# Performance work log

Hardware: AMD Instinct MI355X
Metric: run time of the kernel (lower is better)

Reference implementation:

```python
import jax, jax.numpy as jnp
import numpy as np

EMBED_DIM = 2048
HEAD_DIM = 128


def setup_inputs() -> dict:
    key = jax.random.key(0)
    ks = jax.random.split(key, 7)
    B, S = 4, 2048
    lim = 1.0 / np.sqrt(EMBED_DIM)
    hidden_state = jax.random.normal(ks[0], (B, S, EMBED_DIM), dtype=jnp.float32)
    # nn.Linear weights stored as [out, in]; we keep [in, out] for x @ W
    Wq = jax.random.uniform(ks[1], (EMBED_DIM, HEAD_DIM), minval=-lim, maxval=lim, dtype=jnp.float32)
    Wk = jax.random.uniform(ks[2], (EMBED_DIM, HEAD_DIM), minval=-lim, maxval=lim, dtype=jnp.float32)
    Wv = jax.random.uniform(ks[3], (EMBED_DIM, HEAD_DIM), minval=-lim, maxval=lim, dtype=jnp.float32)
    bq = jax.random.uniform(ks[4], (HEAD_DIM,), minval=-lim, maxval=lim, dtype=jnp.float32)
    bk = jax.random.uniform(ks[5], (HEAD_DIM,), minval=-lim, maxval=lim, dtype=jnp.float32)
    bv = jax.random.uniform(ks[6], (HEAD_DIM,), minval=-lim, maxval=lim, dtype=jnp.float32)
    return {"hidden_state": hidden_state, "Wq": Wq, "bq": bq, "Wk": Wk, "bk": bk, "Wv": Wv, "bv": bv}


def reference(hidden_state, Wq, bq, Wk, bk, Wv, bv):
    q = hidden_state @ Wq + bq  # [B,S,D]
    k = hidden_state @ Wk + bk
    v = hidden_state @ Wv + bv
    scale = 1.0 / jnp.sqrt(jnp.asarray(HEAD_DIM, dtype=q.dtype))
    scores = jnp.einsum("bqd,bkd->bqk", q, k) * scale  # [B,S,S]
    S = q.shape[1]
    causal = jnp.triu(jnp.ones((S, S), dtype=bool), k=1)
    scores = jnp.where(causal, jnp.asarray(-1e10, dtype=scores.dtype), scores)
    weights = jax.nn.softmax(scores, axis=-1)
    return jnp.einsum("bqk,bkd->bqd", weights, v)
```

## Files before the change

### kernel.cpp

```cpp
#include <hip/hip_runtime.h>
#include <hip/hip_bf16.h>

#define EMBED 2048
#define SEQ   2048
#define BATCH 4
#define HD    128
#define MROWS (BATCH * SEQ)
#define NTOT  (3 * HD)
#define SCALE 0.08838834764831845f
#define NQT   (SEQ / 16)
#define NSPL  2
#define FIXM  4.0f

typedef __attribute__((ext_vector_type(8))) short bf16x8;
typedef __attribute__((ext_vector_type(4))) float f32x4;

__device__ __forceinline__ unsigned short f2bf_rne(float x) {
    union { float f; unsigned u; } c; c.f = x;
    unsigned r = c.u + 0x7fffu + ((c.u >> 16) & 1u);
    return (unsigned short)(r >> 16);
}

#define MFMA16(a, b, c) __builtin_amdgcn_mfma_f32_16x16x32_bf16((a), (b), (c), 0, 0, 0)

__device__ __forceinline__ void gload_lds16(const unsigned short* gp, unsigned short* lp) {
    __builtin_amdgcn_global_load_lds(
        (const __attribute__((address_space(1))) void*)gp,
        (__attribute__((address_space(3))) void*)lp, 16, 0, 0);
}

__global__ __launch_bounds__(256) void h_conv(
    const float* __restrict__ H, unsigned short* __restrict__ Hbf)
{
    const size_t i = ((size_t)blockIdx.x * 256 + threadIdx.x) * 8;
    const float4 f0 = *(const float4*)(H + i);
    const float4 f1 = *(const float4*)(H + i + 4);
    union { unsigned short s[8]; uint4 v; } u;
    u.s[0] = f2bf_rne(f0.x); u.s[1] = f2bf_rne(f0.y);
    u.s[2] = f2bf_rne(f0.z); u.s[3] = f2bf_rne(f0.w);
    u.s[4] = f2bf_rne(f1.x); u.s[5] = f2bf_rne(f1.y);
    u.s[6] = f2bf_rne(f1.z); u.s[7] = f2bf_rne(f1.w);
    *(uint4*)(Hbf + i) = u.v;
}

__global__ __launch_bounds__(256) void wt_conv(
    const float* __restrict__ Wq, const float* __restrict__ Wk,
    const float* __restrict__ Wv, unsigned short* __restrict__ WT)
{
    __shared__ float lds[64][129];
    const int tid = threadIdx.x;
    const int blk = blockIdx.x;
    const int mat = blk >> 5;
    const int k0  = (blk & 31) * 64;
    const float* src = (mat == 0) ? Wq : (mat == 1) ? Wk : Wv;

    const float4* s4 = (const float4*)(src + (size_t)k0 * HD);
    for (int i = tid; i < 2048; i += 256) {
        const float4 v = s4[i];
        const int k  = i >> 5;
        const int n4 = (i & 31) * 4;
        lds[k][n4 + 0] = v.x; lds[k][n4 + 1] = v.y;
        lds[k][n4 + 2] = v.z; lds[k][n4 + 3] = v.w;
    }
    __syncthreads();

    const int n  = tid >> 1;
    const int kc = (tid & 1) * 32;
    unsigned short* dst = WT + ((size_t)(mat * HD + n)) * EMBED + k0 + kc;
#pragma unroll
    for (int c = 0; c < 4; ++c) {
        union { unsigned short s[8]; uint4 v; } u;
#pragma unroll
        for (int i = 0; i < 8; ++i)
            u.s[i] = f2bf_rne(lds[kc + c * 8 + i][n]);
        ((uint4*)dst)[c] = u.v;
    }
}

__global__ __launch_bounds__(256, 2) void gemm_qkv(
    const unsigned short* __restrict__ Hbf, const unsigned short* __restrict__ WT,
    const float* __restrict__ bq, const float* __restrict__ bk,
    const float* __restrict__ bv,
    unsigned short* __restrict__ Qbf, unsigned short* __restrict__ Kbf,
    unsigned short* __restrict__ VT)
{
    __shared__ unsigned short Abuf[128 * 64];
    __shared__ unsigned short Bbuf[64 * 64];

    const int tid  = threadIdx.x;
    const int w    = tid >> 6;
    const int lane = tid & 63;
    const int l16  = lane & 15;
    const int quad = lane >> 4;

    const int bid   = blockIdx.x;
    const int xcd   = bid & 7;
    const int local = bid >> 3;
    const int n_blk = local % 6;
    const int m_grp = local / 6;
    const int m0 = (m_grp * 8 + xcd) * 128;
    const int n0 = n_blk * 64;

    const int lr   = lane >> 3;
    const int slot = lane & 7;
    const int gch  = slot ^ lr;
    const unsigned short* ag[4]; unsigned short* al[4];
#pragma unroll
    for (int t = 0; t < 4; ++t) {
        const int r = (w * 4 + t) * 8 + lr;
        ag[t] = Hbf + (size_t)(m0 + r) * EMBED + gch * 8;
        al[t] = Abuf + (w * 4 + t) * 512;
    }
    const unsigned short* bg[2]; unsigned short* bl[2];
#pragma unroll
    for (int t = 0; t < 2; ++t) {
        const int r = (w * 2 + t) * 8 + lr;
        bg[t] = WT + (size_t)(n0 + r) * EMBED + gch * 8;
        bl[t] = Bbuf + (w * 2 + t) * 512;
    }

    const int wm = (w >> 1) * 64;
    const int wn = (w & 1) * 32;
    const int xq = l16 & 7;

    f32x4 acc[4][2];
#pragma unroll
    for (int mt = 0; mt < 4; ++mt)
#pragma unroll
        for (int nt = 0; nt < 2; ++nt) {
            f32x4 z = {0.f, 0.f, 0.f, 0.f};
            acc[mt][nt] = z;
        }

    for (int kt = 0; kt < EMBED / 64; ++kt) {
        const int ko = kt * 64;
#pragma unroll
        for (int t = 0; t < 4; ++t) gload_lds16(ag[t] + ko, al[t]);
#pragma unroll
        for (int t = 0; t < 2; ++t) gload_lds16(bg[t] + ko, bl[t]);
        __syncthreads();

        bf16x8 aF[4][2], bF[2][2];
#pragma unroll
        for (int mt = 0; mt < 4; ++mt)
#pragma unroll
            for (int ks = 0; ks < 2; ++ks)
                aF[mt][ks] = *(const bf16x8*)(
                    Abuf + (wm + mt * 16 + l16) * 64 + (((ks * 4 + quad) ^ xq) * 8));
#pragma unroll
        for (int nt = 0; nt < 2; ++nt)
#pragma unroll
            for (int ks = 0; ks < 2; ++ks)
                bF[nt][ks] = *(const bf16x8*)(
                    Bbuf + (wn + nt * 16 + l16) * 64 + (((ks * 4 + quad) ^ xq) * 8));
#pragma unroll
        for (int ks = 0; ks < 2; ++ks)
#pragma unroll
            for (int mt = 0; mt < 4; ++mt)
#pragma unroll
                for (int nt = 0; nt < 2; ++nt)
                    acc[mt][nt] = MFMA16(aF[mt][ks], bF[nt][ks], acc[mt][nt]);
        __syncthreads();
    }

#pragma unroll
    for (int nt = 0; nt < 2; ++nt) {
        const int col = n0 + wn + nt * 16 + l16;
        const int sel = col >> 7;
        const int c   = col & (HD - 1);
        const float bias = (sel == 0 ? bq : (sel == 1 ? bk : bv))[c];
#pragma unroll
        for (int mt = 0; mt < 4; ++mt) {
#pragma unroll
            for (int r = 0; r < 4; ++r) {
                const int row = m0 + wm + mt * 16 + quad * 4 + r;
                const float v = acc[mt][nt][r] + bias;
                if (sel == 0) {
                    Qbf[(size_t)row * HD + c] = f2bf_rne(v * SCALE);
                } else if (sel == 1) {
                    Kbf[(size_t)row * HD + c] = f2bf_rne(v);
                } else {
                    const int b = row >> 11;
                    const int s = row & (SEQ - 1);
                    VT[((size_t)b * HD + c) * SEQ + s] = f2bf_rne(v);
                }
            }
        }
    }
}

__global__ __launch_bounds__(256, 3) void flash_attn(
    const unsigned short* __restrict__ Qbf,
    const unsigned short* __restrict__ Kbf,
    const unsigned short* __restrict__ VT,
    float* __restrict__ pO, float* __restrict__ pL)
{
    __shared__ unsigned short plds[4][16 * 72];
    __shared__ float obuf[4][16][HD];
    __shared__ float lbuf[4][16];

    const int tid  = threadIdx.x;
    const int w    = tid >> 6;
    const int lane = tid & 63;
    const int l16  = lane & 15;
    const int quad = lane >> 4;
    const int b    = blockIdx.y;
    const int qt    = blockIdx.x >> 1;
    const int split = blockIdx.x & 1;
    const int q0    = (NQT - 1 - qt) * 16;
    const int g     = split * 4 + w;
    const int ntiles = (q0 + 16 + 63) >> 6;
    const int tmax   = (ntiles + 7) >> 3;

    bf16x8 aq[4];
    const unsigned short* qrow = Qbf + ((size_t)b * SEQ + q0 + l16) * HD + quad * 8;
#pragma unroll
    for (int kt = 0; kt < 4; ++kt)
        aq[kt] = *(const bf16x8*)(qrow + kt * 32);

    f32x4 o[8];
#pragma unroll
    for (int nt = 0; nt < 8; ++nt) {
        f32x4 z = {0.f, 0.f, 0.f, 0.f};
        o[nt] = z;
    }
    float l_run[4];
#pragma unroll
    for (int r = 0; r < 4; ++r) l_run[r] = 0.f;

    const unsigned short* kbase = Kbf + (size_t)b * SEQ * HD;
    const unsigned short* vbase = VT + (size_t)b * HD * SEQ;
    unsigned short* myp = &plds[w][0];

    for (int t = 0; t < tmax; ++t) {
        const int tile = t * 8 + g;
        if (tile >= ntiles) continue;
        const int j0 = tile * 64;

        f32x4 s[4];
#pragma unroll
        for (int nt = 0; nt < 4; ++nt) {
            f32x4 z = {0.f, 0.f, 0.f, 0.f};
            s[nt] = z;
        }
#pragma unroll
        for (int kt = 0; kt < 4; ++kt) {
#pragma unroll
            for (int nt = 0; nt < 4; ++nt) {
                const bf16x8 bk = *(const bf16x8*)(
                    kbase + (size_t)(j0 + nt * 16 + l16) * HD + kt * 32 + quad * 8);
                s[nt] = MFMA16(aq[kt], bk, s[nt]);
            }
        }

#pragma unroll
        for (int nt = 0; nt < 4; ++nt) {
            const int j = j0 + nt * 16 + l16;
#pragma unroll
            for (int r = 0; r < 4; ++r) {
                const int q = q0 + quad * 4 + r;
                const float sv = (j > q) ? -1e30f : s[nt][r];
                const float pv = __expf(sv - FIXM);
                l_run[r] += pv;
                myp[(quad * 4 + r) * 72 + nt * 16 + l16] = f2bf_rne(pv);
            }
        }
        asm volatile("s_waitcnt lgkmcnt(0)" ::: "memory");
        const bf16x8 pf0 = *(const bf16x8*)(myp + l16 * 72 + quad * 8);
        const bf16x8 pf1 = *(const bf16x8*)(myp + l16 * 72 + 32 + quad * 8);

#pragma unroll
        for (int nt = 0; nt < 8; ++nt) {
            const bf16x8 bv0 = *(const bf16x8*)(
                vbase + (size_t)(nt * 16 + l16) * SEQ + j0 + quad * 8);
            o[nt] = MFMA16(pf0, bv0, o[nt]);
        }
#pragma unroll
        for (int nt = 0; nt < 8; ++nt) {
            const bf16x8 bv1 = *(const bf16x8*)(
                vbase + (size_t)(nt * 16 + l16) * SEQ + j0 + 32 + quad * 8);
            o[nt] = MFMA16(pf1, bv1, o[nt]);
        }
    }

#pragma unroll
    for (int r = 0; r < 4; ++r) {
#pragma unroll
        for (int d = 1; d < 16; d <<= 1)
            l_run[r] += __shfl_xor(l_run[r], d);
    }
    if (l16 == 0) {
#pragma unroll
        for (int r = 0; r < 4; ++r)
            lbuf[w][quad * 4 + r] = l_run[r];
    }
#pragma unroll
    for (int nt = 0; nt < 8; ++nt)
#pragma unroll
        for (int r = 0; r < 4; ++r)
            obuf[w][quad * 4 + r][nt * 16 + l16] = o[nt][r];
    __syncthreads();

    const int qr = tid >> 4;
    const int d0 = (tid & 15) * 8;
    const int part = ((b * NQT + qt) * NSPL + split);
    float* po = pO + (size_t)part * (16 * HD) + qr * HD + d0;
#pragma unroll
    for (int dd = 0; dd < 8; ++dd) {
        float acc = 0.f;
#pragma unroll
        for (int w2 = 0; w2 < 4; ++w2)
            acc += obuf[w2][qr][d0 + dd];
        po[dd] = acc;
    }
    if ((tid & 15) == 0) {
        pL[part * 16 + qr] =
            lbuf[0][qr] + lbuf[1][qr] + lbuf[2][qr] + lbuf[3][qr];
    }
}

__global__ __launch_bounds__(256) void attn_merge(
    const float* __restrict__ pO, const float* __restrict__ pL,
    float* __restrict__ out)
{
    const int qt = blockIdx.x;
    const int b  = blockIdx.y;
    const int q0 = (NQT - 1 - qt) * 16;
    const int tid = threadIdx.x;
    const int qr = tid >> 4;
    const int d0 = (tid & 15) * 8;
    const int p0 = (b * NQT + qt) * NSPL;

    const float L = pL[p0 * 16 + qr] + pL[(p0 + 1) * 16 + qr];
    const float invL = 1.0f / L;

    const float* o0 = pO + (size_t)p0 * (16 * HD) + qr * HD + d0;
    const float* o1 = o0 + 16 * HD;
    float* op = out + ((size_t)b * SEQ + q0 + qr) * HD + d0;
#pragma unroll
    for (int dd = 0; dd < 8; ++dd)
        op[dd] = (o0[dd] + o1[dd]) * invL;
}

extern "C" void kernel_launch(void* const* d_in, const int* in_sizes, int n_in,
                              void* d_out, int out_size, void* d_ws, size_t ws_size,
                              hipStream_t stream)
{
    const float* h  = (const float*)d_in[0];
    const float* Wq = (const float*)d_in[1];
    const float* bq = (const float*)d_in[2];
    const float* Wk = (const float*)d_in[3];
    const float* bk = (const float*)d_in[4];
    const float* Wv = (const float*)d_in[5];
    const float* bv = (const float*)d_in[6];
    float* out = (float*)d_out;

    unsigned short* Hbf = (unsigned short*)d_ws;
    unsigned short* Qbf = Hbf + (size_t)MROWS * EMBED;
    unsigned short* Kbf = Qbf + (size_t)MROWS * HD;
    unsigned short* VT  = Kbf + (size_t)MROWS * HD;
    unsigned short* WT  = VT  + (size_t)MROWS * HD;
    float* pO  = (float*)d_ws;
    float* pL  = pO + (size_t)BATCH * NQT * NSPL * 16 * HD;

    h_conv<<<(MROWS * EMBED) / (256 * 8), 256, 0, stream>>>(h, Hbf);
    wt_conv<<<96, 256, 0, stream>>>(Wq, Wk, Wv, WT);
    gemm_qkv<<<384, 256, 0, stream>>>(Hbf, WT, bq, bk, bv, Qbf, Kbf, VT);
    flash_attn<<<dim3(NQT * NSPL, BATCH), 256, 0, stream>>>(Qbf, Kbf, VT, pO, pL);
    attn_merge<<<dim3(NQT, BATCH), 256, 0, stream>>>(pO, pL, out);
}
```

Baseline: 193.1 us.

## Share K/V tiles in LDS across four query waves per block

Restructures flash attention so each block handles a 64-row query tile, with each wave owning 16 query rows. K and V key tiles are staged into swizzled LDS through global_load_lds and reused by all four waves, instead of every wave reading K/V from global memory on its own. Key tiles are split across 6 blocks per query tile, and the merge kernel sums the 6 partials. This removes the cross-wave LDS reduction at the end, but adds two barriers per tile and more partial-output traffic in the merge.

```diff
diff --git a/kernel.cpp b/kernel.cpp
--- a/kernel.cpp
+++ b/kernel.cpp
@@ -8,8 +8,8 @@
 #define MROWS (BATCH * SEQ)
 #define NTOT  (3 * HD)
 #define SCALE 0.08838834764831845f
-#define NQT   (SEQ / 16)
-#define NSPL  2
+#define NBQ   (SEQ / 64)
+#define NSPL  6
 #define FIXM  4.0f
 
 typedef __attribute__((ext_vector_type(8))) short bf16x8;
@@ -195,9 +195,9 @@
     const unsigned short* __restrict__ VT,
     float* __restrict__ pO, float* __restrict__ pL)
 {
+    __shared__ unsigned short Kbuf[64 * 128];
+    __shared__ unsigned short Vbuf[128 * 64];
     __shared__ unsigned short plds[4][16 * 72];
-    __shared__ float obuf[4][16][HD];
-    __shared__ float lbuf[4][16];
 
     const int tid  = threadIdx.x;
     const int w    = tid >> 6;
@@ -205,15 +205,13 @@
     const int l16  = lane & 15;
     const int quad = lane >> 4;
     const int b    = blockIdx.y;
-    const int qt    = blockIdx.x >> 1;
-    const int split = blockIdx.x & 1;
-    const int q0    = (NQT - 1 - qt) * 16;
-    const int g     = split * 4 + w;
-    const int ntiles = (q0 + 16 + 63) >> 6;
-    const int tmax   = (ntiles + 7) >> 3;
+    const int qb    = NBQ - 1 - blockIdx.x / NSPL;
+    const int split = blockIdx.x % NSPL;
+    const int q0    = qb * 64;
+    const int qw0   = q0 + w * 16;
 
     bf16x8 aq[4];
-    const unsigned short* qrow = Qbf + ((size_t)b * SEQ + q0 + l16) * HD + quad * 8;
+    const unsigned short* qrow = Qbf + ((size_t)b * SEQ + qw0 + l16) * HD + quad * 8;
 #pragma unroll
     for (int kt = 0; kt < 4; ++kt)
         aq[kt] = *(const bf16x8*)(qrow + kt * 32);
@@ -228,59 +226,76 @@
 #pragma unroll
     for (int r = 0; r < 4; ++r) l_run[r] = 0.f;
 
+    const int lr4 = lane >> 4, sl4 = lane & 15;
+    const int lr8 = lane >> 3, sl8 = lane & 7;
     const unsigned short* kbase = Kbf + (size_t)b * SEQ * HD;
     const unsigned short* vbase = VT + (size_t)b * HD * SEQ;
     unsigned short* myp = &plds[w][0];
 
-    for (int t = 0; t < tmax; ++t) {
-        const int tile = t * 8 + g;
-        if (tile >= ntiles) continue;
-        const int j0 = tile * 64;
-
-        f32x4 s[4];
-#pragma unroll
-        for (int nt = 0; nt < 4; ++nt) {
-            f32x4 z = {0.f, 0.f, 0.f, 0.f};
-            s[nt] = z;
-        }
-#pragma unroll
-        for (int kt = 0; kt < 4; ++kt) {
+    for (int t = split; t <= qb; t += NSPL) {
+        const int j0 = t * 64;
+
+#pragma unroll
+        for (int i = 0; i < 4; ++i) {
+            const int jl = w * 16 + i * 4 + lr4;
+            gload_lds16(kbase + (size_t)(j0 + jl) * HD + (sl4 ^ (i * 4 + lr4)) * 8,
+                        Kbuf + (w * 16 + i * 4) * 128);
+        }
+#pragma unroll
+        for (int i = 0; i < 4; ++i) {
+            const int dr = w * 32 + i * 8 + lr8;
+            gload_lds16(vbase + (size_t)dr * SEQ + j0 + (sl8 ^ lr8) * 8,
+                        Vbuf + (w * 32 + i * 8) * 64);
+        }
+        __syncthreads();
+
+        if (j0 <= qw0 + 15) {
+            f32x4 s[4];
 #pragma unroll
             for (int nt = 0; nt < 4; ++nt) {
-                const bf16x8 bk = *(const bf16x8*)(
-                    kbase + (size_t)(j0 + nt * 16 + l16) * HD + kt * 32 + quad * 8);
-                s[nt] = MFMA16(aq[kt], bk, s[nt]);
-            }
-        }
-
-#pragma unroll
-        for (int nt = 0; nt < 4; ++nt) {
-            const int j = j0 + nt * 16 + l16;
-#pragma unroll
-            for (int r = 0; r < 4; ++r) {
-                const int q = q0 + quad * 4 + r;
-                const float sv = (j > q) ? -1e30f : s[nt][r];
-                const float pv = __expf(sv - FIXM);
-                l_run[r] += pv;
-                myp[(quad * 4 + r) * 72 + nt * 16 + l16] = f2bf_rne(pv);
-            }
-        }
-        asm volatile("s_waitcnt lgkmcnt(0)" ::: "memory");
-        const bf16x8 pf0 = *(const bf16x8*)(myp + l16 * 72 + quad * 8);
-        const bf16x8 pf1 = *(const bf16x8*)(myp + l16 * 72 + 32 + quad * 8);
-
-#pragma unroll
-        for (int nt = 0; nt < 8; ++nt) {
-            const bf16x8 bv0 = *(const bf16x8*)(
-                vbase + (size_t)(nt * 16 + l16) * SEQ + j0 + quad * 8);
-            o[nt] = MFMA16(pf0, bv0, o[nt]);
-        }
-#pragma unroll
-        for (int nt = 0; nt < 8; ++nt) {
-            const bf16x8 bv1 = *(const bf16x8*)(
-                vbase + (size_t)(nt * 16 + l16) * SEQ + j0 + 32 + quad * 8);
-            o[nt] = MFMA16(pf1, bv1, o[nt]);
-        }
+                f32x4 z = {0.f, 0.f, 0.f, 0.f};
+                s[nt] = z;
+            }
+#pragma unroll
+            for (int kt = 0; kt < 4; ++kt) {
+#pragma unroll
+                for (int nt = 0; nt < 4; ++nt) {
+                    const bf16x8 bk = *(const bf16x8*)(
+                        Kbuf + (nt * 16 + l16) * 128 + (((kt * 4 + quad) ^ l16) * 8));
+                    s[nt] = MFMA16(aq[kt], bk, s[nt]);
+                }
+            }
+
+#pragma unroll
+            for (int nt = 0; nt < 4; ++nt) {
+                const int j = j0 + nt * 16 + l16;
+#pragma unroll
+                for (int r = 0; r < 4; ++r) {
+                    const int q = qw0 + quad * 4 + r;
+                    const float sv = (j > q) ? -1e30f : s[nt][r];
+                    const float pv = __expf(sv - FIXM);
+                    l_run[r] += pv;
+                    myp[(quad * 4 + r) * 72 + nt * 16 + l16] = f2bf_rne(pv);
+                }
+            }
+            asm volatile("s_waitcnt lgkmcnt(0)" ::: "memory");
+            const bf16x8 pf0 = *(const bf16x8*)(myp + l16 * 72 + quad * 8);
+            const bf16x8 pf1 = *(const bf16x8*)(myp + l16 * 72 + 32 + quad * 8);
+
+#pragma unroll
+            for (int nt = 0; nt < 8; ++nt) {
+                const bf16x8 bv0 = *(const bf16x8*)(
+                    Vbuf + (nt * 16 + l16) * 64 + ((quad ^ (l16 & 7)) * 8));
+                o[nt] = MFMA16(pf0, bv0, o[nt]);
+            }
+#pragma unroll
+            for (int nt = 0; nt < 8; ++nt) {
+                const bf16x8 bv1 = *(const bf16x8*)(
+                    Vbuf + (nt * 16 + l16) * 64 + (((4 + quad) ^ (l16 & 7)) * 8));
+                o[nt] = MFMA16(pf1, bv1, o[nt]);
+            }
+        }
+        __syncthreads();
     }
 
 #pragma unroll
@@ -289,33 +304,17 @@
         for (int d = 1; d < 16; d <<= 1)
             l_run[r] += __shfl_xor(l_run[r], d);
     }
+    const int part = (b * NBQ + qb) * NSPL + split;
+    float* po = pO + (size_t)part * (64 * HD);
+#pragma unroll
+    for (int nt = 0; nt < 8; ++nt)
+#pragma unroll
+        for (int r = 0; r < 4; ++r)
+            po[(w * 16 + quad * 4 + r) * HD + nt * 16 + l16] = o[nt][r];
     if (l16 == 0) {
 #pragma unroll
         for (int r = 0; r < 4; ++r)
-            lbuf[w][quad * 4 + r] = l_run[r];
-    }
-#pragma unroll
-    for (int nt = 0; nt < 8; ++nt)
-#pragma unroll
-        for (int r = 0; r < 4; ++r)
-            obuf[w][quad * 4 + r][nt * 16 + l16] = o[nt][r];
-    __syncthreads();
-
-    const int qr = tid >> 4;
-    const int d0 = (tid & 15) * 8;
-    const int part = ((b * NQT + qt) * NSPL + split);
-    float* po = pO + (size_t)part * (16 * HD) + qr * HD + d0;
-#pragma unroll
-    for (int dd = 0; dd < 8; ++dd) {
-        float acc = 0.f;
-#pragma unroll
-        for (int w2 = 0; w2 < 4; ++w2)
-            acc += obuf[w2][qr][d0 + dd];
-        po[dd] = acc;
-    }
-    if ((tid & 15) == 0) {
-        pL[part * 16 + qr] =
-            lbuf[0][qr] + lbuf[1][qr] + lbuf[2][qr] + lbuf[3][qr];
+            pL[part * 64 + w * 16 + quad * 4 + r] = l_run[r];
     }
 }
 
@@ -323,23 +322,33 @@
     const float* __restrict__ pO, const float* __restrict__ pL,
     float* __restrict__ out)
 {
-    const int qt = blockIdx.x;
+    const int qb = blockIdx.x;
     const int b  = blockIdx.y;
-    const int q0 = (NQT - 1 - qt) * 16;
     const int tid = threadIdx.x;
-    const int qr = tid >> 4;
-    const int d0 = (tid & 15) * 8;
-    const int p0 = (b * NQT + qt) * NSPL;
-
-    const float L = pL[p0 * 16 + qr] + pL[(p0 + 1) * 16 + qr];
+    const int r  = tid >> 2;
+    const int d0 = (tid & 3) * 32;
+    const int p0 = (b * NBQ + qb) * NSPL;
+
+    float L = 0.f;
+#pragma unroll
+    for (int s = 0; s < NSPL; ++s) L += pL[(p0 + s) * 64 + r];
     const float invL = 1.0f / L;
 
-    const float* o0 = pO + (size_t)p0 * (16 * HD) + qr * HD + d0;
-    const float* o1 = o0 + 16 * HD;
-    float* op = out + ((size_t)b * SEQ + q0 + qr) * HD + d0;
-#pragma unroll
-    for (int dd = 0; dd < 8; ++dd)
-        op[dd] = (o0[dd] + o1[dd]) * invL;
+    float* op = out + ((size_t)b * SEQ + qb * 64 + r) * HD + d0;
+#pragma unroll
+    for (int c = 0; c < 8; ++c) {
+        float4 acc = {0.f, 0.f, 0.f, 0.f};
+#pragma unroll
+        for (int s = 0; s < NSPL; ++s) {
+            const float4 v = *(const float4*)(
+                pO + (size_t)(p0 + s) * (64 * HD) + r * HD + d0 + c * 4);
+            acc.x += v.x; acc.y += v.y; acc.z += v.z; acc.w += v.w;
+        }
+        op[c * 4 + 0] = acc.x * invL;
+        op[c * 4 + 1] = acc.y * invL;
+        op[c * 4 + 2] = acc.z * invL;
+        op[c * 4 + 3] = acc.w * invL;
+    }
 }
 
 extern "C" void kernel_launch(void* const* d_in, const int* in_sizes, int n_in,
@@ -361,11 +370,11 @@
     unsigned short* VT  = Kbf + (size_t)MROWS * HD;
     unsigned short* WT  = VT  + (size_t)MROWS * HD;
     float* pO  = (float*)d_ws;
-    float* pL  = pO + (size_t)BATCH * NQT * NSPL * 16 * HD;
+    float* pL  = pO + (size_t)BATCH * NBQ * NSPL * 64 * HD;
 
     h_conv<<<(MROWS * EMBED) / (256 * 8), 256, 0, stream>>>(h, Hbf);
     wt_conv<<<96, 256, 0, stream>>>(Wq, Wk, Wv, WT);
     gemm_qkv<<<384, 256, 0, stream>>>(Hbf, WT, bq, bk, bv, Qbf, Kbf, VT);
-    flash_attn<<<dim3(NQT * NSPL, BATCH), 256, 0, stream>>>(Qbf, Kbf, VT, pO, pL);
-    attn_merge<<<dim3(NQT, BATCH), 256, 0, stream>>>(pO, pL, out);
-}
+    flash_attn<<<dim3(NBQ * NSPL, BATCH), 256, 0, stream>>>(Qbf, Kbf, VT, pO, pL);
+    attn_merge<<<dim3(NBQ, BATCH), 256, 0, stream>>>(pO, pL, out);
+}
```

After: 173.3 us. -10.2%, faster.
